# Kernel optimization log

Measured on AMD Instinct MI355X. Metric: run time of the kernel, lower is better.

## Reference

```python
import jax, jax.numpy as jnp
import numpy as np

N = 50000
E = 800000
F_IN = 128
H = 64
C = 10
BN_EPS = 1e-5


def _glorot(key, shape):
    fan_in = shape[0]
    return jax.random.normal(key, shape, dtype=jnp.float32) / jnp.sqrt(jnp.float32(fan_in))


def setup_inputs() -> dict:
    key = jax.random.key(0)
    ks = jax.random.split(key, 16)
    inp = {
        "x": jax.random.normal(ks[0], (N, F_IN), dtype=jnp.float32),
        "edge_index": jax.random.randint(ks[1], (2, E), 0, N, dtype=jnp.int64),
    }
    # GINConv layer params: eps (train_eps=True, init 0), 2-layer MLP, BN affine
    dims = [(F_IN, H), (H, H), (H, H)]
    for i, (din, dout) in enumerate(dims, start=1):
        k1, k2 = jax.random.split(ks[1 + i], 2)
        inp[f"eps{i}"] = jnp.float32(0.0)
        inp[f"w{i}a"] = _glorot(k1, (din, H))
        inp[f"b{i}a"] = jnp.zeros((H,), jnp.float32)
        inp[f"w{i}b"] = _glorot(k2, (H, H))
        inp[f"b{i}b"] = jnp.zeros((H,), jnp.float32)
        inp[f"g{i}"] = jnp.ones((H,), jnp.float32)
        inp[f"be{i}"] = jnp.zeros((H,), jnp.float32)
    inp["lin_w"] = _glorot(ks[10], (H, C))
    inp["lin_b"] = jnp.zeros((C,), jnp.float32)
    return inp


def _gin_conv(x, src, dst, eps, wa, ba, wb, bb, g, be):
    # sum-aggregate neighbor features: scatter-add x[src] into dst rows
    agg = jax.ops.segment_sum(x[src], dst, num_segments=N)
    h = (1.0 + eps) * x + agg
    # MLP: Linear-ReLU-Linear-ReLU-BatchNorm1d (training-mode batch stats)
    h = jax.nn.relu(h @ wa + ba)
    h = jax.nn.relu(h @ wb + bb)
    mean = jnp.mean(h, axis=0)
    var = jnp.var(h, axis=0)
    return (h - mean) * jax.lax.rsqrt(var + BN_EPS) * g + be


def reference(x, edge_index,
              eps1, w1a, b1a, w1b, b1b, g1, be1,
              eps2, w2a, b2a, w2b, b2b, g2, be2,
              eps3, w3a, b3a, w3b, b3b, g3, be3,
              lin_w, lin_b):
    src, dst = edge_index[0], edge_index[1]
    h = jax.nn.relu(_gin_conv(x, src, dst, eps1, w1a, b1a, w1b, b1b, g1, be1))
    h = jax.nn.relu(_gin_conv(h, src, dst, eps2, w2a, b2a, w2b, b2b, g2, be2))
    h = jax.nn.relu(_gin_conv(h, src, dst, eps3, w3a, b3a, w3b, b3b, g3, be3))
    return h @ lin_w + lin_b
```

## Files before the change

kernel.cpp:

```cpp
#include <hip/hip_runtime.h>
#include <hip/hip_fp16.h>

#define NN 50000
#define NGROUP 3125
#define NCHUNK 391
#define CHCAP 3072
#define SLAB 8192
#define BN_EPS 1e-5f

typedef unsigned int uint;
typedef unsigned short ushort;
typedef _Float16 half8 __attribute__((ext_vector_type(8)));
typedef float floatx4 __attribute__((ext_vector_type(4)));

__device__ __forceinline__ int aswz(int slot) { return slot ^ ((slot >> 4) & 7); }

__device__ __forceinline__ float h_lo(uint u) {
    return __half2float(__ushort_as_half((ushort)(u & 0xFFFFu)));
}
__device__ __forceinline__ float h_hi(uint u) {
    return __half2float(__ushort_as_half((ushort)(u >> 16)));
}
__device__ __forceinline__ void unpack8(uint4 v, float* f) {
    f[0] = h_lo(v.x); f[1] = h_hi(v.x);
    f[2] = h_lo(v.y); f[3] = h_hi(v.y);
    f[4] = h_lo(v.z); f[5] = h_hi(v.z);
    f[6] = h_lo(v.w); f[7] = h_hi(v.w);
}

__global__ __launch_bounds__(256) void sortA_kernel(
    const int* __restrict__ ei, int* __restrict__ gcur,
    uint* __restrict__ bucket, int E)
{
    __shared__ int s_hist[NCHUNK];
    __shared__ int s_offs[NCHUNK];
    __shared__ int s_cur[NCHUNK];
    __shared__ int s_gb[NCHUNK];
    __shared__ int s_scanA[512], s_scanB[512];
    __shared__ uint s_sorted[SLAB];

    const int tid  = threadIdx.x;
    const int base = blockIdx.x * SLAB;
    const int cnt  = min(SLAB, E - base);

    for (int i = tid; i < NCHUNK; i += 256) s_hist[i] = 0;
    __syncthreads();

    uint pk[SLAB / 256];
    int nloc = 0;
    for (int i = tid; i < cnt; i += 256) {
        int src = ei[base + i];
        int dst = ei[E + base + i];
        int c = dst >> 7;
        pk[nloc++] = (uint)src | ((uint)(dst & 127) << 16) | ((uint)c << 23);
        atomicAdd(&s_hist[c], 1);
    }
    __syncthreads();
    for (int i = tid; i < 512; i += 256) s_scanA[i] = (i < NCHUNK) ? s_hist[i] : 0;
    __syncthreads();
    int* sa = s_scanA; int* sb = s_scanB;
    for (int off = 1; off < 512; off <<= 1) {
        for (int i = tid; i < 512; i += 256)
            sb[i] = sa[i] + ((i >= off) ? sa[i - off] : 0);
        __syncthreads();
        int* t = sa; sa = sb; sb = t;
    }
    for (int i = tid; i < NCHUNK; i += 256) {
        int excl = sa[i] - s_hist[i];
        s_offs[i] = excl;
        s_cur[i]  = excl;
    }
    __syncthreads();
    for (int k = 0; k < nloc; k++) {
        int c = pk[k] >> 23;
        int pos = atomicAdd(&s_cur[c], 1);
        s_sorted[pos] = pk[k];
    }
    __syncthreads();
    for (int c = tid; c < NCHUNK; c += 256) {
        int n = s_hist[c];
        s_gb[c] = n ? atomicAdd(&gcur[c], n) : 0;
    }
    __syncthreads();
    for (int i = tid; i < cnt; i += 256) {
        uint v = s_sorted[i];
        int c = v >> 23;
        int li = i - s_offs[c];
        bucket[(size_t)c * CHCAP + s_gb[c] + li] = v;
    }
}

__global__ __launch_bounds__(256) void chunk_scan_kernel(
    const int* __restrict__ gcur, int* __restrict__ chunkBase,
    int* __restrict__ rowPtr, int E)
{
    __shared__ int sA[512], sB[512];
    const int tid = threadIdx.x;
    for (int i = tid; i < 512; i += 256) sA[i] = (i < NCHUNK) ? gcur[i] : 0;
    __syncthreads();
    int* sa = sA; int* sb = sB;
    for (int off = 1; off < 512; off <<= 1) {
        for (int i = tid; i < 512; i += 256)
            sb[i] = sa[i] + ((i >= off) ? sa[i - off] : 0);
        __syncthreads();
        int* t = sa; sa = sb; sb = t;
    }
    for (int i = tid; i < NCHUNK; i += 256)
        chunkBase[i] = sa[i] - gcur[i];
    if (tid == 0) rowPtr[NN] = E;
}

__global__ __launch_bounds__(256) void fillB_kernel(
    const uint* __restrict__ bucket, const int* __restrict__ gcur,
    const int* __restrict__ chunkBase,
    int* __restrict__ rowPtr, int* __restrict__ csr_src)
{
    __shared__ int s_hist[128];
    __shared__ int s_excl[128];
    __shared__ int s_cur[128];
    const int c = blockIdx.x;
    const int tid = threadIdx.x;
    const int cnt = gcur[c];
    const int row0 = c * 128;
    const int base = chunkBase[c];

    if (tid < 128) s_hist[tid] = 0;
    __syncthreads();
    for (int i = tid; i < cnt; i += 256) {
        uint v = bucket[(size_t)c * CHCAP + i];
        atomicAdd(&s_hist[(v >> 16) & 127], 1);
    }
    __syncthreads();
    if (tid < 128) {
        int lane = tid & 63;
        int v = s_hist[tid];
        int incl = v;
        #pragma unroll
        for (int off = 1; off < 64; off <<= 1) {
            int t = __shfl_up(incl, off, 64);
            if (lane >= off) incl += t;
        }
        s_excl[tid] = incl - v;
    }
    __syncthreads();
    if (tid < 128) {
        int excl = s_excl[tid];
        if (tid >= 64) excl += s_excl[63] + s_hist[63];
        s_excl[tid] = excl;
        s_cur[tid] = excl;
        int row = row0 + tid;
        if (row < NN) rowPtr[row] = base + excl;
    }
    __syncthreads();
    for (int i = tid; i < cnt; i += 256) {
        uint v = bucket[(size_t)c * CHCAP + i];
        int dl  = (v >> 16) & 127;
        int src = v & 0xFFFFu;
        int ofs = atomicAdd(&s_cur[dl], 1);
        csr_src[base + ofs] = src;
    }
}

template<int FIN, bool APPLY>
__global__ __launch_bounds__(256, 4) void proj_kernel(
    const void* __restrict__ in_v,
    const float* __restrict__ stats_in, const float* __restrict__ g_in,
    const float* __restrict__ be_in,
    const float* __restrict__ wa,
    ushort* __restrict__ y_out)
{
    constexpr int KC = FIN / 32;
    __shared__ __align__(16) _Float16 s_B[FIN * 64];
    __shared__ __align__(16) _Float16 s_Y[4][1024];

    const int tid = threadIdx.x, w = tid >> 6, lane = tid & 63;
    const int q = lane >> 4, mm = lane & 15;

    for (int i = tid; i < FIN * 64; i += 256) {
        int j = i & 7, l = (i >> 3) & 63, t = i >> 9;
        int kc = t >> 2, nt = t & 3;
        int k = kc * 32 + (l >> 4) * 8 + j;
        int n = nt * 16 + (l & 15);
        s_B[i] = (_Float16)wa[k * 64 + n];
    }

    float scv[2][8], shv[2][8];
    if (APPLY) {
        #pragma unroll
        for (int kc = 0; kc < 2; kc++)
            #pragma unroll
            for (int j = 0; j < 8; j++) {
                int c = kc * 32 + q * 8 + j;
                float mean = stats_in[c] * (1.0f / NN);
                float var  = stats_in[64 + c] * (1.0f / NN) - mean * mean;
                float rstd = rsqrtf(var + BN_EPS);
                float s    = rstd * g_in[c];
                scv[kc][j] = s;
                shv[kc][j] = be_in[c] - mean * s;
            }
    }
    __syncthreads();

    int g = blockIdx.x * 4 + w;
    if (g >= NGROUP) return;
    const int row = g * 16 + mm;

    half8 af[KC];
    if (FIN == 128) {
        const float* xin = (const float*)in_v;
        #pragma unroll
        for (int kc = 0; kc < KC; kc++) {
            const float* p = xin + (size_t)row * 128 + kc * 32 + q * 8;
            float4 a = *(const float4*)p;
            float4 b = *(const float4*)(p + 4);
            half8 hv;
            hv[0] = (_Float16)a.x; hv[1] = (_Float16)a.y;
            hv[2] = (_Float16)a.z; hv[3] = (_Float16)a.w;
            hv[4] = (_Float16)b.x; hv[5] = (_Float16)b.y;
            hv[6] = (_Float16)b.z; hv[7] = (_Float16)b.w;
            af[kc] = hv;
        }
    } else {
        const ushort* hin = (const ushort*)in_v;
        #pragma unroll
        for (int kc = 0; kc < KC; kc++) {
            uint4 vv = *(const uint4*)(hin + (size_t)row * 64 + kc * 32 + q * 8);
            float f[8]; unpack8(vv, f);
            half8 hv;
            #pragma unroll
            for (int j = 0; j < 8; j++) {
                float z = APPLY ? fmaxf(fmaf(f[j], scv[kc][j], shv[kc][j]), 0.0f) : f[j];
                hv[j] = (_Float16)z;
            }
            af[kc] = hv;
        }
    }

    floatx4 acc[4] = {};
    #pragma unroll
    for (int nt = 0; nt < 4; nt++)
        #pragma unroll
        for (int kc = 0; kc < KC; kc++) {
            half8 bf = *(const half8*)(s_B + ((size_t)(kc * 4 + nt) * 64 + lane) * 8);
            acc[nt] = __builtin_amdgcn_mfma_f32_16x16x32_f16(af[kc], bf, acc[nt], 0, 0, 0);
        }

    _Float16* s_Yw = &s_Y[w][0];
    #pragma unroll
    for (int nt = 0; nt < 4; nt++)
        #pragma unroll
        for (int r = 0; r < 4; r++)
            s_Yw[(q * 4 + r) * 64 + nt * 16 + mm] = (_Float16)acc[nt][r];
    half8 t0 = *(const half8*)(s_Yw + lane * 8);
    half8 t1 = *(const half8*)(s_Yw + 512 + lane * 8);
    half8* dst = (half8*)((_Float16*)y_out + (size_t)g * 1024);
    dst[lane] = t0;
    dst[64 + lane] = t1;
}

__global__ __launch_bounds__(512, 4) void gin_gather_kernel(
    const ushort* __restrict__ y,
    const int* __restrict__ rowPtr, const int* __restrict__ csr_src,
    const float* __restrict__ eps_p, const float* __restrict__ ba,
    const float* __restrict__ wb, const float* __restrict__ bb,
    ushort* __restrict__ h_out, float* __restrict__ stats_out)
{
    __shared__ __align__(16) _Float16 s_B2[64 * 64];
    __shared__ __align__(16) _Float16 s_A[8][1024];
    __shared__ float s_red[8][64];

    const int tid = threadIdx.x, w = tid >> 6, lane = tid & 63;
    const int cc = lane & 7, gph = lane >> 3;
    const int q = lane >> 4, mm = lane & 15;

    for (int i = tid; i < 64 * 64; i += 512) {
        int j = i & 7, l = (i >> 3) & 63, t = i >> 9;
        int kc = t >> 2, nt = t & 3;
        int k = kc * 32 + (l >> 4) * 8 + j;
        int n = nt * 16 + (l & 15);
        s_B2[i] = (_Float16)wb[k * 64 + n];
    }

    const float eps1 = 1.0f + eps_p[0];
    float bav[8];
    #pragma unroll
    for (int j = 0; j < 8; j++) bav[j] = ba[8 * cc + j];
    float bbv[4];
    #pragma unroll
    for (int nt = 0; nt < 4; nt++) bbv[nt] = bb[nt * 16 + mm];
    __syncthreads();

    float bn_s[4] = {0.f, 0.f, 0.f, 0.f};
    float bn_q[4] = {0.f, 0.f, 0.f, 0.f};
    const uint4* y4 = (const uint4*)y;
    const int g = blockIdx.x * 8 + w;

    if (g < NGROUP) {
        const int row0 = g * 16;
        _Float16* s_Aw = &s_A[w][0];

        for (int m = 0; m < 16; m += 4) {
            int e[4], en[4], s[4];
            float a[4][8];
            uint4 v[4];
            #pragma unroll
            for (int i = 0; i < 4; i++) {
                int row = row0 + m + i;
                e[i] = rowPtr[row] + gph;
                en[i] = rowPtr[row + 1];
                #pragma unroll
                for (int j = 0; j < 8; j++) a[i][j] = 0.0f;
            }
            if (gph == 0) {
                #pragma unroll
                for (int i = 0; i < 4; i++) {
                    uint4 sv = y4[(size_t)(row0 + m + i) * 8 + cc];
                    float f[8]; unpack8(sv, f);
                    #pragma unroll
                    for (int j = 0; j < 8; j++) a[i][j] = eps1 * f[j];
                }
            }
            #pragma unroll
            for (int i = 0; i < 4; i++) s[i] = (e[i] < en[i]) ? csr_src[e[i]] : -1;
            #pragma unroll
            for (int i = 0; i < 4; i++) if (s[i] >= 0) v[i] = y4[(size_t)s[i] * 8 + cc];

            int mx = max(max(s[0], s[1]), max(s[2], s[3]));
            while (mx >= 0) {
                int n[4]; uint4 p[4];
                #pragma unroll
                for (int i = 0; i < 4; i++) {
                    n[i] = -1;
                    if (s[i] >= 0) { e[i] += 8; n[i] = (e[i] < en[i]) ? csr_src[e[i]] : -1; }
                }
                #pragma unroll
                for (int i = 0; i < 4; i++) if (n[i] >= 0) p[i] = y4[(size_t)n[i] * 8 + cc];
                #pragma unroll
                for (int i = 0; i < 4; i++) {
                    if (s[i] >= 0) {
                        float f[8]; unpack8(v[i], f);
                        #pragma unroll
                        for (int j = 0; j < 8; j++) a[i][j] += f[j];
                    }
                    s[i] = n[i]; v[i] = p[i];
                }
                mx = max(max(s[0], s[1]), max(s[2], s[3]));
            }

            #pragma unroll
            for (int off = 8; off < 64; off <<= 1)
                #pragma unroll
                for (int i = 0; i < 4; i++)
                    #pragma unroll
                    for (int j = 0; j < 8; j++)
                        a[i][j] += __shfl_xor(a[i][j], off, 64);

            if (gph == 0) {
                #pragma unroll
                for (int i = 0; i < 4; i++) {
                    half8 hv;
                    #pragma unroll
                    for (int j = 0; j < 8; j++)
                        hv[j] = (_Float16)fmaxf(a[i][j] + bav[j], 0.0f);
                    int slot = (cc >> 2) * 64 + (cc & 3) * 16 + (m + i);
                    *(half8*)(s_Aw + (size_t)aswz(slot) * 8) = hv;
                }
            }
        }

        half8 af2[2];
        #pragma unroll
        for (int kc = 0; kc < 2; kc++)
            af2[kc] = *(const half8*)(s_Aw + (size_t)aswz(kc * 64 + lane) * 8);
        floatx4 acc2[4] = {};
        #pragma unroll
        for (int nt = 0; nt < 4; nt++)
            #pragma unroll
            for (int kc = 0; kc < 2; kc++) {
                half8 bf = *(const half8*)(s_B2 + ((size_t)(kc * 4 + nt) * 64 + lane) * 8);
                acc2[nt] = __builtin_amdgcn_mfma_f32_16x16x32_f16(af2[kc], bf, acc2[nt], 0, 0, 0);
            }

        #pragma unroll
        for (int nt = 0; nt < 4; nt++)
            #pragma unroll
            for (int r = 0; r < 4; r++) {
                float val = fmaxf(acc2[nt][r] + bbv[nt], 0.0f);
                bn_s[nt] += val;
                bn_q[nt] += val * val;
                s_Aw[(q * 4 + r) * 64 + nt * 16 + mm] = (_Float16)val;
            }
        half8 t0 = *(const half8*)(s_Aw + lane * 8);
        half8 t1 = *(const half8*)(s_Aw + 512 + lane * 8);
        half8* dst = (half8*)((_Float16*)h_out + (size_t)row0 * 64);
        dst[lane] = t0;
        dst[64 + lane] = t1;
    }

    #pragma unroll
    for (int nt = 0; nt < 4; nt++) {
        bn_s[nt] += __shfl_xor(bn_s[nt], 16, 64);
        bn_s[nt] += __shfl_xor(bn_s[nt], 32, 64);
        bn_q[nt] += __shfl_xor(bn_q[nt], 16, 64);
        bn_q[nt] += __shfl_xor(bn_q[nt], 32, 64);
    }
    __syncthreads();
    if (lane < 16) {
        #pragma unroll
        for (int nt = 0; nt < 4; nt++) s_red[w][nt * 16 + lane] = bn_s[nt];
    }
    __syncthreads();
    if (w == 0) {
        float s = 0;
        #pragma unroll
        for (int j = 0; j < 8; j++) s += s_red[j][lane];
        atomicAdd(&stats_out[lane], s);
    }
    __syncthreads();
    if (lane < 16) {
        #pragma unroll
        for (int nt = 0; nt < 4; nt++) s_red[w][nt * 16 + lane] = bn_q[nt];
    }
    __syncthreads();
    if (w == 0) {
        float s = 0;
        #pragma unroll
        for (int j = 0; j < 8; j++) s += s_red[j][lane];
        atomicAdd(&stats_out[64 + lane], s);
    }
}

__global__ __launch_bounds__(256) void final_linear_kernel(
    const ushort* __restrict__ h, const float* __restrict__ stats,
    const float* __restrict__ g, const float* __restrict__ be,
    const float* __restrict__ w, const float* __restrict__ b,
    float* __restrict__ out)
{
    __shared__ float s_w[640];
    __shared__ float s_b[10];
    __shared__ float s_scale[64];
    __shared__ float s_shift[64];
    for (int i = threadIdx.x; i < 640; i += 256) s_w[i] = w[i];
    if (threadIdx.x < 10) s_b[threadIdx.x] = b[threadIdx.x];
    if (threadIdx.x < 64) {
        int c = threadIdx.x;
        float mean = stats[c] * (1.0f / NN);
        float var  = stats[64 + c] * (1.0f / NN) - mean * mean;
        float rstd = rsqrtf(var + BN_EPS);
        float s    = rstd * g[c];
        s_scale[c] = s;
        s_shift[c] = be[c] - mean * s;
    }
    __syncthreads();
    int row = blockIdx.x * 256 + threadIdx.x;
    if (row >= NN) return;
    float acc[10];
    #pragma unroll
    for (int c = 0; c < 10; c++) acc[c] = s_b[c];
    const uint4* hr = (const uint4*)(h + (size_t)row * 64);
    #pragma unroll
    for (int ch = 0; ch < 8; ch++) {
        uint4 v = hr[ch];
        float f[8]; unpack8(v, f);
        #pragma unroll
        for (int j = 0; j < 8; j++) {
            int k = ch * 8 + j;
            float val = fmaxf(fmaf(f[j], s_scale[k], s_shift[k]), 0.0f);
            #pragma unroll
            for (int c = 0; c < 10; c++) acc[c] = fmaf(val, s_w[k * 10 + c], acc[c]);
        }
    }
    #pragma unroll
    for (int c = 0; c < 10; c++) out[row * 10 + c] = acc[c];
}

extern "C" void kernel_launch(void* const* d_in, const int* in_sizes, int n_in,
                              void* d_out, int out_size, void* d_ws, size_t ws_size,
                              hipStream_t stream)
{
    const float* x  = (const float*)d_in[0];
    const int*   ei = (const int*)d_in[1];
    const int E = in_sizes[1] / 2;

    const float* eps[3]; const float* wa[3]; const float* ba[3];
    const float* wb[3];  const float* bb[3]; const float* g[3]; const float* be[3];
    for (int i = 0; i < 3; i++) {
        int base = 2 + 7 * i;
        eps[i] = (const float*)d_in[base + 0];
        wa[i]  = (const float*)d_in[base + 1];
        ba[i]  = (const float*)d_in[base + 2];
        wb[i]  = (const float*)d_in[base + 3];
        bb[i]  = (const float*)d_in[base + 4];
        g[i]   = (const float*)d_in[base + 5];
        be[i]  = (const float*)d_in[base + 6];
    }
    const float* lin_w = (const float*)d_in[23];
    const float* lin_b = (const float*)d_in[24];
    float* out = (float*)d_out;

    char*  base   = (char*)d_ws;
    int*   gcur   = (int*)base;
    int*   chunkB = gcur + 512;
    int*   rowPtr = chunkB + 512;
    uint*  bucket = (uint*)(rowPtr + NN + 1);
    int*   csrsrc = (int*)(bucket + (size_t)NCHUNK * CHCAP);
    size_t ioff   = (char*)(csrsrc + E) - base;
    ushort* yb    = (ushort*)(base + ((ioff + 15) & ~(size_t)15));
    ushort* hA    = yb + (size_t)NN * 64;
    ushort* hB    = hA + (size_t)NN * 64;
    float* stats  = (float*)(hB + (size_t)NN * 64);

    hipMemsetAsync(gcur, 0, 512 * sizeof(int), stream);
    hipMemsetAsync(stats, 0, 3 * 128 * sizeof(float), stream);
    sortA_kernel<<<(E + SLAB - 1) / SLAB, 256, 0, stream>>>(ei, gcur, bucket, E);
    chunk_scan_kernel<<<1, 256, 0, stream>>>(gcur, chunkB, rowPtr, E);
    fillB_kernel<<<NCHUNK, 256, 0, stream>>>(bucket, gcur, chunkB, rowPtr, csrsrc);

    const int PB = (NGROUP + 3) / 4;
    const int GB = (NGROUP + 7) / 8;

    proj_kernel<128, false><<<PB, 256, 0, stream>>>(
        x, nullptr, nullptr, nullptr, wa[0], yb);
    gin_gather_kernel<<<GB, 512, 0, stream>>>(
        yb, rowPtr, csrsrc, eps[0], ba[0], wb[0], bb[0], hA, stats);
    proj_kernel<64, true><<<PB, 256, 0, stream>>>(
        hA, stats, g[0], be[0], wa[1], yb);
    gin_gather_kernel<<<GB, 512, 0, stream>>>(
        yb, rowPtr, csrsrc, eps[1], ba[1], wb[1], bb[1], hB, stats + 128);
    proj_kernel<64, true><<<PB, 256, 0, stream>>>(
        hB, stats + 128, g[1], be[1], wa[2], yb);
    gin_gather_kernel<<<GB, 512, 0, stream>>>(
        yb, rowPtr, csrsrc, eps[2], ba[2], wb[2], bb[2], hA, stats + 256);
    final_linear_kernel<<<(NN + 255) / 256, 256, 0, stream>>>(
        hA, stats + 256, g[2], be[2], lin_w, lin_b, out);
}
```

Before: 313.0 us.

## Split gather groups across wave pairs, fold chunk scan into fill, shrink sort slabs

Several changes at once. The gather kernel now assigns each 16-row group to two waves, each gathering 8 rows and computing half of the second-layer output columns. This doubles the block count and raises the occupancy hint to increase parallelism on the latency-bound neighbor gather. The separate chunk-scan kernel is removed, and each fillB block computes its own prefix base by summing the preceding chunk counts. The sort slab size is reduced to launch more sortA blocks. The trade-off is extra block-level syncs and some redundant prefix summation per block.

```diff
diff --git a/kernel.cpp b/kernel.cpp
--- a/kernel.cpp
+++ b/kernel.cpp
@@ -5,7 +5,7 @@
 #define NGROUP 3125
 #define NCHUNK 391
 #define CHCAP 3072
-#define SLAB 8192
+#define SLAB 2048
 #define BN_EPS 1e-5f
 
 typedef unsigned int uint;
@@ -90,42 +90,32 @@
     }
 }
 
-__global__ __launch_bounds__(256) void chunk_scan_kernel(
-    const int* __restrict__ gcur, int* __restrict__ chunkBase,
-    int* __restrict__ rowPtr, int E)
-{
-    __shared__ int sA[512], sB[512];
-    const int tid = threadIdx.x;
-    for (int i = tid; i < 512; i += 256) sA[i] = (i < NCHUNK) ? gcur[i] : 0;
-    __syncthreads();
-    int* sa = sA; int* sb = sB;
-    for (int off = 1; off < 512; off <<= 1) {
-        for (int i = tid; i < 512; i += 256)
-            sb[i] = sa[i] + ((i >= off) ? sa[i - off] : 0);
-        __syncthreads();
-        int* t = sa; sa = sb; sb = t;
-    }
-    for (int i = tid; i < NCHUNK; i += 256)
-        chunkBase[i] = sa[i] - gcur[i];
-    if (tid == 0) rowPtr[NN] = E;
-}
-
 __global__ __launch_bounds__(256) void fillB_kernel(
     const uint* __restrict__ bucket, const int* __restrict__ gcur,
-    const int* __restrict__ chunkBase,
     int* __restrict__ rowPtr, int* __restrict__ csr_src)
 {
     __shared__ int s_hist[128];
     __shared__ int s_excl[128];
     __shared__ int s_cur[128];
+    __shared__ int s_ws[4];
+    __shared__ int s_base;
     const int c = blockIdx.x;
     const int tid = threadIdx.x;
     const int cnt = gcur[c];
     const int row0 = c * 128;
-    const int base = chunkBase[c];
-
+
+    int part = 0;
+    for (int i = tid; i < c; i += 256) part += gcur[i];
+    #pragma unroll
+    for (int off = 32; off >= 1; off >>= 1) part += __shfl_down(part, off, 64);
+    if ((tid & 63) == 0) s_ws[tid >> 6] = part;
     if (tid < 128) s_hist[tid] = 0;
     __syncthreads();
+    if (tid == 0) s_base = s_ws[0] + s_ws[1] + s_ws[2] + s_ws[3];
+    __syncthreads();
+    const int base = s_base;
+    if (tid == 0 && c == NCHUNK - 1) rowPtr[NN] = base + cnt;
+
     for (int i = tid; i < cnt; i += 256) {
         uint v = bucket[(size_t)c * CHCAP + i];
         atomicAdd(&s_hist[(v >> 16) & 127], 1);
@@ -146,7 +136,6 @@
     if (tid < 128) {
         int excl = s_excl[tid];
         if (tid >= 64) excl += s_excl[63] + s_hist[63];
-        s_excl[tid] = excl;
         s_cur[tid] = excl;
         int row = row0 + tid;
         if (row < NN) rowPtr[row] = base + excl;
@@ -258,7 +247,7 @@
     dst[64 + lane] = t1;
 }
 
-__global__ __launch_bounds__(512, 4) void gin_gather_kernel(
+__global__ __launch_bounds__(512, 6) void gin_gather_kernel(
     const ushort* __restrict__ y,
     const int* __restrict__ rowPtr, const int* __restrict__ csr_src,
     const float* __restrict__ eps_p, const float* __restrict__ ba,
@@ -266,10 +255,12 @@
     ushort* __restrict__ h_out, float* __restrict__ stats_out)
 {
     __shared__ __align__(16) _Float16 s_B2[64 * 64];
-    __shared__ __align__(16) _Float16 s_A[8][1024];
-    __shared__ float s_red[8][64];
+    __shared__ __align__(16) _Float16 s_A[4][1024];
+    __shared__ __align__(16) _Float16 s_T[4][1024];
+    __shared__ float s_red[8][32];
 
     const int tid = threadIdx.x, w = tid >> 6, lane = tid & 63;
+    const int p = w >> 1, sub = w & 1;
     const int cc = lane & 7, gph = lane >> 3;
     const int q = lane >> 4, mm = lane & 15;
 
@@ -285,27 +276,29 @@
     float bav[8];
     #pragma unroll
     for (int j = 0; j < 8; j++) bav[j] = ba[8 * cc + j];
-    float bbv[4];
-    #pragma unroll
-    for (int nt = 0; nt < 4; nt++) bbv[nt] = bb[nt * 16 + mm];
-    __syncthreads();
-
-    float bn_s[4] = {0.f, 0.f, 0.f, 0.f};
-    float bn_q[4] = {0.f, 0.f, 0.f, 0.f};
+    float bbv[2];
+    #pragma unroll
+    for (int ntl = 0; ntl < 2; ntl++) bbv[ntl] = bb[(sub * 2 + ntl) * 16 + mm];
+    __syncthreads();
+
+    const int g = blockIdx.x * 4 + p;
+    const bool active = g < NGROUP;
+    const int row0 = g * 16;
+    float bn_s[2] = {0.f, 0.f};
+    float bn_q[2] = {0.f, 0.f};
     const uint4* y4 = (const uint4*)y;
-    const int g = blockIdx.x * 8 + w;
-
-    if (g < NGROUP) {
-        const int row0 = g * 16;
-        _Float16* s_Aw = &s_A[w][0];
-
-        for (int m = 0; m < 16; m += 4) {
+    _Float16* s_Ap = &s_A[p][0];
+    _Float16* s_Tp = &s_T[p][0];
+
+    if (active) {
+        for (int mb = 0; mb < 8; mb += 4) {
+            const int m0 = sub * 8 + mb;
             int e[4], en[4], s[4];
             float a[4][8];
             uint4 v[4];
             #pragma unroll
             for (int i = 0; i < 4; i++) {
-                int row = row0 + m + i;
+                int row = row0 + m0 + i;
                 e[i] = rowPtr[row] + gph;
                 en[i] = rowPtr[row + 1];
                 #pragma unroll
@@ -314,7 +307,7 @@
             if (gph == 0) {
                 #pragma unroll
                 for (int i = 0; i < 4; i++) {
-                    uint4 sv = y4[(size_t)(row0 + m + i) * 8 + cc];
+                    uint4 sv = y4[(size_t)(row0 + m0 + i) * 8 + cc];
                     float f[8]; unpack8(sv, f);
                     #pragma unroll
                     for (int j = 0; j < 8; j++) a[i][j] = eps1 * f[j];
@@ -327,14 +320,14 @@
 
             int mx = max(max(s[0], s[1]), max(s[2], s[3]));
             while (mx >= 0) {
-                int n[4]; uint4 p[4];
+                int n[4]; uint4 pf[4];
                 #pragma unroll
                 for (int i = 0; i < 4; i++) {
                     n[i] = -1;
                     if (s[i] >= 0) { e[i] += 8; n[i] = (e[i] < en[i]) ? csr_src[e[i]] : -1; }
                 }
                 #pragma unroll
-                for (int i = 0; i < 4; i++) if (n[i] >= 0) p[i] = y4[(size_t)n[i] * 8 + cc];
+                for (int i = 0; i < 4; i++) if (n[i] >= 0) pf[i] = y4[(size_t)n[i] * 8 + cc];
                 #pragma unroll
                 for (int i = 0; i < 4; i++) {
                     if (s[i] >= 0) {
@@ -342,7 +335,7 @@
                         #pragma unroll
                         for (int j = 0; j < 8; j++) a[i][j] += f[j];
                     }
-                    s[i] = n[i]; v[i] = p[i];
+                    s[i] = n[i]; v[i] = pf[i];
                 }
                 mx = max(max(s[0], s[1]), max(s[2], s[3]));
             }
@@ -362,70 +355,77 @@
                     #pragma unroll
                     for (int j = 0; j < 8; j++)
                         hv[j] = (_Float16)fmaxf(a[i][j] + bav[j], 0.0f);
-                    int slot = (cc >> 2) * 64 + (cc & 3) * 16 + (m + i);
-                    *(half8*)(s_Aw + (size_t)aswz(slot) * 8) = hv;
+                    int slot = (cc >> 2) * 64 + (cc & 3) * 16 + (m0 + i);
+                    *(half8*)(s_Ap + (size_t)aswz(slot) * 8) = hv;
                 }
             }
         }
-
+    }
+    __syncthreads();
+
+    if (active) {
         half8 af2[2];
         #pragma unroll
         for (int kc = 0; kc < 2; kc++)
-            af2[kc] = *(const half8*)(s_Aw + (size_t)aswz(kc * 64 + lane) * 8);
-        floatx4 acc2[4] = {};
-        #pragma unroll
-        for (int nt = 0; nt < 4; nt++)
+            af2[kc] = *(const half8*)(s_Ap + (size_t)aswz(kc * 64 + lane) * 8);
+        floatx4 acc2[2] = {};
+        #pragma unroll
+        for (int ntl = 0; ntl < 2; ntl++) {
+            int nt = sub * 2 + ntl;
             #pragma unroll
             for (int kc = 0; kc < 2; kc++) {
                 half8 bf = *(const half8*)(s_B2 + ((size_t)(kc * 4 + nt) * 64 + lane) * 8);
-                acc2[nt] = __builtin_amdgcn_mfma_f32_16x16x32_f16(af2[kc], bf, acc2[nt], 0, 0, 0);
-            }
-
-        #pragma unroll
-        for (int nt = 0; nt < 4; nt++)
+                acc2[ntl] = __builtin_amdgcn_mfma_f32_16x16x32_f16(af2[kc], bf, acc2[ntl], 0, 0, 0);
+            }
+        }
+        #pragma unroll
+        for (int ntl = 0; ntl < 2; ntl++)
             #pragma unroll
             for (int r = 0; r < 4; r++) {
-                float val = fmaxf(acc2[nt][r] + bbv[nt], 0.0f);
-                bn_s[nt] += val;
-                bn_q[nt] += val * val;
-                s_Aw[(q * 4 + r) * 64 + nt * 16 + mm] = (_Float16)val;
-            }
-        half8 t0 = *(const half8*)(s_Aw + lane * 8);
-        half8 t1 = *(const half8*)(s_Aw + 512 + lane * 8);
-        half8* dst = (half8*)((_Float16*)h_out + (size_t)row0 * 64);
-        dst[lane] = t0;
-        dst[64 + lane] = t1;
-    }
-
-    #pragma unroll
-    for (int nt = 0; nt < 4; nt++) {
-        bn_s[nt] += __shfl_xor(bn_s[nt], 16, 64);
-        bn_s[nt] += __shfl_xor(bn_s[nt], 32, 64);
-        bn_q[nt] += __shfl_xor(bn_q[nt], 16, 64);
-        bn_q[nt] += __shfl_xor(bn_q[nt], 32, 64);
+                float val = fmaxf(acc2[ntl][r] + bbv[ntl], 0.0f);
+                bn_s[ntl] += val;
+                bn_q[ntl] += val * val;
+                s_Tp[(q * 4 + r) * 64 + (sub * 2 + ntl) * 16 + mm] = (_Float16)val;
+            }
+    }
+    __syncthreads();
+
+    if (active) {
+        half8 t = *(const half8*)(s_Tp + sub * 512 + (size_t)lane * 8);
+        ((half8*)((_Float16*)h_out + (size_t)g * 1024))[sub * 64 + lane] = t;
+    }
+
+    #pragma unroll
+    for (int ntl = 0; ntl < 2; ntl++) {
+        bn_s[ntl] += __shfl_xor(bn_s[ntl], 16, 64);
+        bn_s[ntl] += __shfl_xor(bn_s[ntl], 32, 64);
+        bn_q[ntl] += __shfl_xor(bn_q[ntl], 16, 64);
+        bn_q[ntl] += __shfl_xor(bn_q[ntl], 32, 64);
     }
     __syncthreads();
     if (lane < 16) {
-        #pragma unroll
-        for (int nt = 0; nt < 4; nt++) s_red[w][nt * 16 + lane] = bn_s[nt];
+        s_red[w][lane]      = bn_s[0];
+        s_red[w][16 + lane] = bn_s[1];
     }
     __syncthreads();
     if (w == 0) {
+        int sn = lane >> 5, lc = lane & 31;
         float s = 0;
         #pragma unroll
-        for (int j = 0; j < 8; j++) s += s_red[j][lane];
+        for (int j = 0; j < 4; j++) s += s_red[2 * j + sn][lc];
         atomicAdd(&stats_out[lane], s);
     }
     __syncthreads();
     if (lane < 16) {
-        #pragma unroll
-        for (int nt = 0; nt < 4; nt++) s_red[w][nt * 16 + lane] = bn_q[nt];
+        s_red[w][lane]      = bn_q[0];
+        s_red[w][16 + lane] = bn_q[1];
     }
     __syncthreads();
     if (w == 0) {
+        int sn = lane >> 5, lc = lane & 31;
         float s = 0;
         #pragma unroll
-        for (int j = 0; j < 8; j++) s += s_red[j][lane];
+        for (int j = 0; j < 4; j++) s += s_red[2 * j + sn][lc];
         atomicAdd(&stats_out[64 + lane], s);
     }
 }
@@ -500,8 +500,7 @@
 
     char*  base   = (char*)d_ws;
     int*   gcur   = (int*)base;
-    int*   chunkB = gcur + 512;
-    int*   rowPtr = chunkB + 512;
+    int*   rowPtr = gcur + 512;
     uint*  bucket = (uint*)(rowPtr + NN + 1);
     int*   csrsrc = (int*)(bucket + (size_t)NCHUNK * CHCAP);
     size_t ioff   = (char*)(csrsrc + E) - base;
@@ -513,11 +512,10 @@
     hipMemsetAsync(gcur, 0, 512 * sizeof(int), stream);
     hipMemsetAsync(stats, 0, 3 * 128 * sizeof(float), stream);
     sortA_kernel<<<(E + SLAB - 1) / SLAB, 256, 0, stream>>>(ei, gcur, bucket, E);
-    chunk_scan_kernel<<<1, 256, 0, stream>>>(gcur, chunkB, rowPtr, E);
-    fillB_kernel<<<NCHUNK, 256, 0, stream>>>(bucket, gcur, chunkB, rowPtr, csrsrc);
+    fillB_kernel<<<NCHUNK, 256, 0, stream>>>(bucket, gcur, rowPtr, csrsrc);
 
     const int PB = (NGROUP + 3) / 4;
-    const int GB = (NGROUP + 7) / 8;
+    const int GB = (NGROUP + 3) / 4;
 
     proj_kernel<128, false><<<PB, 256, 0, stream>>>(
         x, nullptr, nullptr, nullptr, wa[0], yb);
```

After: 503.7 us. +60.9%, slower.
